# Kernel tuning notes

Hardware: AMD Instinct MI355X
Metric: run time of the kernel (lower is better)

Reference implementation:

```python
import jax, jax.numpy as jnp
import numpy as np


def _mlp(h, W_in, b_in, W_hid, b_hid, W_out, b_out):
    # 392 -> 1000 -> (1000)x4 -> 392, ReLU between linear layers (NICE shift net)
    h = jax.nn.relu(h @ W_in + b_in)
    for i in range(W_hid.shape[0]):  # fixed small layer count, not a data dim
        h = jax.nn.relu(h @ W_hid[i] + b_hid[i])
    return h @ W_out + b_out


def setup_inputs() -> dict:
    key = jax.random.key(0)
    ks = jax.random.split(key, 4)
    B, D, MID = 4096, 784, 1000
    half = D // 2
    return {
        "x": jax.random.normal(ks[0], (B, D), jnp.float32),
        "log_det_J": jnp.zeros((1,), jnp.float32),
        "W_in": jax.random.normal(ks[1], (half, MID), jnp.float32) * 0.05,
        "b_in": jnp.zeros((MID,), jnp.float32),
        "W_hid": jax.random.normal(ks[2], (4, MID, MID), jnp.float32) * 0.03,
        "b_hid": jnp.zeros((4, MID), jnp.float32),
        "W_out": jax.random.normal(ks[3], (MID, half), jnp.float32) * 0.03,
        "b_out": jnp.zeros((half,), jnp.float32),
    }


def reference(x, log_det_J, W_in, b_in, W_hid, b_hid, W_out, b_out):
    # mask_config = 0: first = even columns, second = odd columns
    first = x[:, 0::2]   # (B, D/2)
    second = x[:, 1::2]  # (B, D/2)
    shift = _mlp(first, W_in, b_in, W_hid, b_hid, W_out, b_out)
    y_second = second + shift  # coupling_law (reverse=False)
    # interleave: y[:, 0::2] = first, y[:, 1::2] = y_second, in one strided write
    y = jnp.stack([first, y_second], axis=2).reshape(x.shape)
    return (y, log_det_J)
```

## Files before the change

### kernel.cpp

```cpp
#include <hip/hip_runtime.h>

typedef __bf16 bf16;
typedef __bf16 bf16x8 __attribute__((ext_vector_type(8)));
typedef float f32x4 __attribute__((ext_vector_type(4)));

#define M_TOT 4096
#define D_IN  784
#define HALF  392
#define MID   1000
#define K0PAD 448
#define NPAD  1024
#define N5PAD 512

__device__ __forceinline__ void g2l16(const bf16* g, bf16* l) {
  __builtin_amdgcn_global_load_lds(
      (__attribute__((address_space(1))) void*)(g),
      (__attribute__((address_space(3))) void*)(l),
      16, 0, 0);
}

__global__ void prep_k(const float* __restrict__ x, const float* __restrict__ ldj,
                       const float* __restrict__ W_in, const float* __restrict__ W_hid,
                       const float* __restrict__ W_out,
                       bf16* __restrict__ A0, bf16* __restrict__ WT0,
                       bf16* __restrict__ WTh, bf16* __restrict__ WT5,
                       float* __restrict__ y) {
  int b = blockIdx.x;
  int tid = threadIdx.x;
  if (b == 0 && tid == 0) y[(size_t)M_TOT * D_IN] = ldj[0];

  if (b < 8192) {
    int m = b >> 1;
    int k = (b & 1) * 256 + tid;
    if (k < K0PAD)
      A0[(size_t)m * K0PAD + k] = (k < HALF) ? (bf16)x[(size_t)m * D_IN + 2 * k] : (bf16)0.f;
    return;
  }
  int t = b - 8192;
  const float* W; bf16* WT; int K, N, Kpad, tn, tk;
  if (t < 448) {
    W = W_in; WT = WT0; K = HALF; N = MID; Kpad = K0PAD;
    tn = t & 31; tk = t >> 5;
  } else if (t < 448 + 4096) {
    int u = t - 448; int i = u >> 10; u &= 1023;
    W = W_hid + (size_t)i * MID * MID; WT = WTh + (size_t)i * NPAD * NPAD;
    K = MID; N = MID; Kpad = NPAD;
    tn = u & 31; tk = u >> 5;
  } else {
    int u = t - 4544;
    W = W_out; WT = WT5; K = MID; N = HALF; Kpad = NPAD;
    tn = u & 15; tk = u >> 4;
  }
  __shared__ float tb[32][33];
  int n0 = tn * 32, k0 = tk * 32;
  int tx = tid & 31, ty = tid >> 5;
#pragma unroll
  for (int r = 0; r < 4; ++r) {
    int k = k0 + ty + 8 * r, n = n0 + tx;
    tb[ty + 8 * r][tx] = (k < K && n < N) ? W[(size_t)k * N + n] : 0.f;
  }
  __syncthreads();
#pragma unroll
  for (int r = 0; r < 4; ++r) {
    int n = n0 + ty + 8 * r, k = k0 + tx;
    WT[(size_t)n * Kpad + k] = (bf16)tb[tx][ty + 8 * r];
  }
}

template <int BM, int BN, int EPI, int K>
__global__ __launch_bounds__(256, 2)
void gemm_k(const bf16* __restrict__ A, const bf16* __restrict__ BT,
            const float* __restrict__ bias, int bias_n,
            bf16* __restrict__ C,
            const float* __restrict__ x, float* __restrict__ y) {
  constexpr int BK = 64;
  constexpr int MT = BM / 32, NT = BN / 32;
  constexpr int KT = K / BK;
  __shared__ bf16 ldsA[BM * BK];
  __shared__ bf16 ldsB[BN * BK];
  const int tid = threadIdx.x, wave = tid >> 6, lane = tid & 63;
  const int bn = blockIdx.x, bm = blockIdx.y;

  const int srow = lane >> 3;
  const int sq = (lane & 7) ^ srow;
  const bf16* gA = A + ((size_t)bm * BM + wave * (BM / 4) + srow) * K + sq * 8;
  const bf16* gB = BT + ((size_t)bn * BN + wave * (BN / 4) + srow) * K + sq * 8;
  bf16* lA = &ldsA[wave * (BM / 4) * BK];
  bf16* lB = &ldsB[wave * (BN / 4) * BK];

  const int mlane = lane & 15, quad = lane >> 4;
  const int wm = (wave & 1) * (BM / 2), wn = (wave >> 1) * (BN / 2);
  const int axor = mlane & 7;
  const bf16* raBase = &ldsA[(wm + mlane) * BK];
  const bf16* rbBase = &ldsB[(wn + mlane) * BK];

  f32x4 acc[MT][NT] = {};

#pragma unroll
  for (int i = 0; i < BM / 32; ++i) g2l16(gA + (size_t)(8 * i) * K, lA + (8 * i) * BK);
#pragma unroll
  for (int i = 0; i < BN / 32; ++i) g2l16(gB + (size_t)(8 * i) * K, lB + (8 * i) * BK);

  for (int kt = 0; kt < KT; ++kt) {
    __syncthreads();
    bf16x8 af[2][MT], bfr[2][NT];
#pragma unroll
    for (int s = 0; s < 2; ++s) {
      const int co = ((s * 4 + quad) ^ axor) * 8;
#pragma unroll
      for (int i = 0; i < MT; ++i) af[s][i] = *(const bf16x8*)(raBase + i * 16 * BK + co);
#pragma unroll
      for (int i = 0; i < NT; ++i) bfr[s][i] = *(const bf16x8*)(rbBase + i * 16 * BK + co);
    }
    __syncthreads();
    if (kt + 1 < KT) {
      const size_t off = (size_t)(kt + 1) * BK;
#pragma unroll
      for (int i = 0; i < BM / 32; ++i) g2l16(gA + off + (size_t)(8 * i) * K, lA + (8 * i) * BK);
#pragma unroll
      for (int i = 0; i < BN / 32; ++i) g2l16(gB + off + (size_t)(8 * i) * K, lB + (8 * i) * BK);
    }
#pragma unroll
    for (int s = 0; s < 2; ++s)
#pragma unroll
      for (int mt = 0; mt < MT; ++mt)
#pragma unroll
        for (int nt = 0; nt < NT; ++nt)
          acc[mt][nt] = __builtin_amdgcn_mfma_f32_16x16x32_bf16(
              af[s][mt], bfr[s][nt], acc[mt][nt], 0, 0, 0);
  }

  const int ng0 = bn * BN + wn + mlane;
  const int mg0 = bm * BM + wm + quad * 4;

  if (EPI == 0) {
    float bv[NT];
#pragma unroll
    for (int nt = 0; nt < NT; ++nt) {
      int n = ng0 + nt * 16;
      bv[nt] = (n < bias_n) ? bias[n] : 0.f;
    }
#pragma unroll
    for (int mt = 0; mt < MT; ++mt)
#pragma unroll
      for (int nt = 0; nt < NT; ++nt)
#pragma unroll
        for (int r = 0; r < 4; ++r) {
          int m = mg0 + mt * 16 + r;
          int n = ng0 + nt * 16;
          float v = fmaxf(acc[mt][nt][r] + bv[nt], 0.f);
          C[(size_t)m * NPAD + n] = (bf16)v;
        }
  } else {
    const float2* x2 = (const float2*)x;
    float2* y2 = (float2*)y;
#pragma unroll
    for (int nt = 0; nt < NT; ++nt) {
      int n = ng0 + nt * 16;
      if (n < HALF) {
        float bb = bias[n];
#pragma unroll
        for (int mt = 0; mt < MT; ++mt)
#pragma unroll
          for (int r = 0; r < 4; ++r) {
            int m = mg0 + mt * 16 + r;
            size_t off = (size_t)m * (D_IN / 2) + n;
            float2 v = x2[off];
            v.y += acc[mt][nt][r] + bb;
            y2[off] = v;
          }
      }
    }
  }
}

extern "C" void kernel_launch(void* const* d_in, const int* in_sizes, int n_in,
                              void* d_out, int out_size, void* d_ws, size_t ws_size,
                              hipStream_t stream) {
  const float* x     = (const float*)d_in[0];
  const float* ldj   = (const float*)d_in[1];
  const float* W_in  = (const float*)d_in[2];
  const float* b_in  = (const float*)d_in[3];
  const float* W_hid = (const float*)d_in[4];
  const float* b_hid = (const float*)d_in[5];
  const float* W_out = (const float*)d_in[6];
  const float* b_out = (const float*)d_in[7];
  float* y = (float*)d_out;

  char* p = (char*)d_ws;
  bf16* A0  = (bf16*)(p + 0);
  bf16* H0  = (bf16*)(p + 3670016);
  bf16* H1  = (bf16*)(p + 12058624);
  bf16* WT0 = (bf16*)(p + 20447232);
  bf16* WTh = (bf16*)(p + 21364736);
  bf16* WT5 = (bf16*)(p + 29753344);

  prep_k<<<dim3(8192 + 5056), 256, 0, stream>>>(x, ldj, W_in, W_hid, W_out,
                                                A0, WT0, WTh, WT5, y);

  gemm_k<64, 128, 0, K0PAD><<<dim3(8, 64), 256, 0, stream>>>(A0, WT0, b_in, MID, H0, nullptr, nullptr);
  gemm_k<64, 128, 0, NPAD><<<dim3(8, 64), 256, 0, stream>>>(H0, WTh + 0 * (size_t)NPAD * NPAD, b_hid + 0 * MID, MID, H1, nullptr, nullptr);
  gemm_k<64, 128, 0, NPAD><<<dim3(8, 64), 256, 0, stream>>>(H1, WTh + 1 * (size_t)NPAD * NPAD, b_hid + 1 * MID, MID, H0, nullptr, nullptr);
  gemm_k<64, 128, 0, NPAD><<<dim3(8, 64), 256, 0, stream>>>(H0, WTh + 2 * (size_t)NPAD * NPAD, b_hid + 2 * MID, MID, H1, nullptr, nullptr);
  gemm_k<64, 128, 0, NPAD><<<dim3(8, 64), 256, 0, stream>>>(H1, WTh + 3 * (size_t)NPAD * NPAD, b_hid + 3 * MID, MID, H0, nullptr, nullptr);
  gemm_k<64, 64, 1, NPAD><<<dim3(8, 64), 256, 0, stream>>>(H0, WT5, b_out, HALF, nullptr, x, y);
}
```

Before: 183.9 us.

## Fuse prep and six GEMM layers into one persistent kernel with row-group barriers

Replaces the prep kernel and six separate GEMM launches with a single persistent kernel of 512 blocks. Weight transposition and input packing run first, followed by a grid-wide barrier. Each later layer is separated only by an 8-block barrier over the blocks that share the same 64-row M slice, since a row tile depends only on its own rows of the previous activation. This removes launch gaps and full-grid drains between layers, but relies on all 512 blocks being co-resident, adds atomic spin barriers plus a memset launch, and loses the larger prep grid's parallelism.

```diff
diff --git a/kernel.cpp b/kernel.cpp
--- a/kernel.cpp
+++ b/kernel.cpp
@@ -10,7 +10,7 @@
 #define MID   1000
 #define K0PAD 448
 #define NPAD  1024
-#define N5PAD 512
+#define NBLK  512
 
 __device__ __forceinline__ void g2l16(const bf16* g, bf16* l) {
   __builtin_amdgcn_global_load_lds(
@@ -19,67 +19,32 @@
       16, 0, 0);
 }
 
-__global__ void prep_k(const float* __restrict__ x, const float* __restrict__ ldj,
-                       const float* __restrict__ W_in, const float* __restrict__ W_hid,
-                       const float* __restrict__ W_out,
-                       bf16* __restrict__ A0, bf16* __restrict__ WT0,
-                       bf16* __restrict__ WTh, bf16* __restrict__ WT5,
-                       float* __restrict__ y) {
-  int b = blockIdx.x;
-  int tid = threadIdx.x;
-  if (b == 0 && tid == 0) y[(size_t)M_TOT * D_IN] = ldj[0];
-
-  if (b < 8192) {
-    int m = b >> 1;
-    int k = (b & 1) * 256 + tid;
-    if (k < K0PAD)
-      A0[(size_t)m * K0PAD + k] = (k < HALF) ? (bf16)x[(size_t)m * D_IN + 2 * k] : (bf16)0.f;
-    return;
-  }
-  int t = b - 8192;
-  const float* W; bf16* WT; int K, N, Kpad, tn, tk;
-  if (t < 448) {
-    W = W_in; WT = WT0; K = HALF; N = MID; Kpad = K0PAD;
-    tn = t & 31; tk = t >> 5;
-  } else if (t < 448 + 4096) {
-    int u = t - 448; int i = u >> 10; u &= 1023;
-    W = W_hid + (size_t)i * MID * MID; WT = WTh + (size_t)i * NPAD * NPAD;
-    K = MID; N = MID; Kpad = NPAD;
-    tn = u & 31; tk = u >> 5;
-  } else {
-    int u = t - 4544;
-    W = W_out; WT = WT5; K = MID; N = HALF; Kpad = NPAD;
-    tn = u & 15; tk = u >> 4;
-  }
-  __shared__ float tb[32][33];
-  int n0 = tn * 32, k0 = tk * 32;
-  int tx = tid & 31, ty = tid >> 5;
-#pragma unroll
-  for (int r = 0; r < 4; ++r) {
-    int k = k0 + ty + 8 * r, n = n0 + tx;
-    tb[ty + 8 * r][tx] = (k < K && n < N) ? W[(size_t)k * N + n] : 0.f;
-  }
+__device__ __forceinline__ void sync_group(unsigned* cnt, unsigned* flag, unsigned nb) {
   __syncthreads();
-#pragma unroll
-  for (int r = 0; r < 4; ++r) {
-    int n = n0 + ty + 8 * r, k = k0 + tx;
-    WT[(size_t)n * Kpad + k] = (bf16)tb[tx][ty + 8 * r];
-  }
-}
-
-template <int BM, int BN, int EPI, int K>
-__global__ __launch_bounds__(256, 2)
-void gemm_k(const bf16* __restrict__ A, const bf16* __restrict__ BT,
-            const float* __restrict__ bias, int bias_n,
-            bf16* __restrict__ C,
-            const float* __restrict__ x, float* __restrict__ y) {
-  constexpr int BK = 64;
+  if (threadIdx.x == 0) {
+    __threadfence();
+    unsigned a = __hip_atomic_fetch_add(cnt, 1u, __ATOMIC_ACQ_REL, __HIP_MEMORY_SCOPE_AGENT);
+    if (a == nb - 1u) {
+      __hip_atomic_store(flag, 1u, __ATOMIC_RELEASE, __HIP_MEMORY_SCOPE_AGENT);
+    } else {
+      while (__hip_atomic_load(flag, __ATOMIC_ACQUIRE, __HIP_MEMORY_SCOPE_AGENT) == 0u)
+        __builtin_amdgcn_s_sleep(2);
+    }
+    __threadfence();
+  }
+  __syncthreads();
+}
+
+template <int K, int BN, int EPI>
+__device__ __forceinline__ void gemm_tile(
+    const bf16* __restrict__ A, const bf16* __restrict__ BT,
+    const float* __restrict__ bias, int bias_n,
+    bf16* __restrict__ C, const float* __restrict__ x, float* __restrict__ y,
+    int bm, int bn, bf16* ldsA, bf16* ldsB) {
+  constexpr int BM = 64, BK = 64;
   constexpr int MT = BM / 32, NT = BN / 32;
   constexpr int KT = K / BK;
-  __shared__ bf16 ldsA[BM * BK];
-  __shared__ bf16 ldsB[BN * BK];
   const int tid = threadIdx.x, wave = tid >> 6, lane = tid & 63;
-  const int bn = blockIdx.x, bm = blockIdx.y;
 
   const int srow = lane >> 3;
   const int sq = (lane & 7) ^ srow;
@@ -172,6 +137,84 @@
       }
     }
   }
+}
+
+__global__ __launch_bounds__(256, 2)
+void fused_k(const float* __restrict__ x, const float* __restrict__ ldj,
+             const float* __restrict__ W_in, const float* __restrict__ b_in,
+             const float* __restrict__ W_hid, const float* __restrict__ b_hid,
+             const float* __restrict__ W_out, const float* __restrict__ b_out,
+             bf16* __restrict__ A0, bf16* __restrict__ WT0,
+             bf16* __restrict__ WTh, bf16* __restrict__ WT5,
+             bf16* __restrict__ H0, bf16* __restrict__ H1,
+             float* __restrict__ y, unsigned* __restrict__ bar) {
+  __shared__ __align__(16) union {
+    struct { bf16 A[64 * 64]; bf16 B[128 * 64]; } g;
+    float tb[32][33];
+  } sm;
+  const int b = blockIdx.x, tid = threadIdx.x;
+
+  if (b == 0 && tid == 0) y[(size_t)M_TOT * D_IN] = ldj[0];
+
+#pragma unroll
+  for (int r = 0; r < 8; ++r) {
+    int m = b * 8 + r;
+    for (int k = tid; k < K0PAD; k += 256)
+      A0[(size_t)m * K0PAD + k] =
+          (k < HALF) ? (bf16)x[(size_t)m * D_IN + 2 * k] : (bf16)0.f;
+  }
+  for (int i = 0; i < 10; ++i) {
+    int t = b + i * NBLK;
+    const float* W = nullptr; bf16* WT = nullptr;
+    int K = 0, N = 0, Kpad = 0, tn = 0, tk = 0;
+    if (t < 448) {
+      W = W_in; WT = WT0; K = HALF; N = MID; Kpad = K0PAD; tn = t & 31; tk = t >> 5;
+    } else if (t < 4544) {
+      int u = t - 448, wi = u >> 10; u &= 1023;
+      W = W_hid + (size_t)wi * MID * MID; WT = WTh + (size_t)wi * NPAD * NPAD;
+      K = MID; N = MID; Kpad = NPAD; tn = u & 31; tk = u >> 5;
+    } else if (t < 5056) {
+      int u = t - 4544;
+      W = W_out; WT = WT5; K = MID; N = HALF; Kpad = NPAD; tn = u & 15; tk = u >> 4;
+    }
+    int tx = tid & 31, ty = tid >> 5;
+    if (W) {
+      int n0 = tn * 32, k0 = tk * 32;
+#pragma unroll
+      for (int r = 0; r < 4; ++r) {
+        int k = k0 + ty + 8 * r, n = n0 + tx;
+        sm.tb[ty + 8 * r][tx] = (k < K && n < N) ? W[(size_t)k * N + n] : 0.f;
+      }
+    }
+    __syncthreads();
+    if (W) {
+      int n0 = tn * 32, k0 = tk * 32;
+#pragma unroll
+      for (int r = 0; r < 4; ++r) {
+        int n = n0 + ty + 8 * r, k = k0 + tx;
+        WT[(size_t)n * Kpad + k] = (bf16)sm.tb[tx][ty + 8 * r];
+      }
+    }
+    __syncthreads();
+  }
+
+  sync_group(&bar[0], &bar[1], NBLK);
+
+  const int bm = b & 63, bn = b >> 6;
+  bf16* ldsA = sm.g.A;
+  bf16* ldsB = sm.g.B;
+
+  gemm_tile<K0PAD, 128, 0>(A0, WT0, b_in, MID, H0, nullptr, nullptr, bm, bn, ldsA, ldsB);
+  sync_group(&bar[2 + 2 * (0 * 64 + bm)], &bar[3 + 2 * (0 * 64 + bm)], 8);
+  gemm_tile<NPAD, 128, 0>(H0, WTh + 0 * (size_t)NPAD * NPAD, b_hid + 0 * MID, MID, H1, nullptr, nullptr, bm, bn, ldsA, ldsB);
+  sync_group(&bar[2 + 2 * (1 * 64 + bm)], &bar[3 + 2 * (1 * 64 + bm)], 8);
+  gemm_tile<NPAD, 128, 0>(H1, WTh + 1 * (size_t)NPAD * NPAD, b_hid + 1 * MID, MID, H0, nullptr, nullptr, bm, bn, ldsA, ldsB);
+  sync_group(&bar[2 + 2 * (2 * 64 + bm)], &bar[3 + 2 * (2 * 64 + bm)], 8);
+  gemm_tile<NPAD, 128, 0>(H0, WTh + 2 * (size_t)NPAD * NPAD, b_hid + 2 * MID, MID, H1, nullptr, nullptr, bm, bn, ldsA, ldsB);
+  sync_group(&bar[2 + 2 * (3 * 64 + bm)], &bar[3 + 2 * (3 * 64 + bm)], 8);
+  gemm_tile<NPAD, 128, 0>(H1, WTh + 3 * (size_t)NPAD * NPAD, b_hid + 3 * MID, MID, H0, nullptr, nullptr, bm, bn, ldsA, ldsB);
+  sync_group(&bar[2 + 2 * (4 * 64 + bm)], &bar[3 + 2 * (4 * 64 + bm)], 8);
+  gemm_tile<NPAD, 64, 1>(H0, WT5, b_out, HALF, nullptr, x, y, bm, bn, ldsA, ldsB);
 }
 
 extern "C" void kernel_launch(void* const* d_in, const int* in_sizes, int n_in,
@@ -188,20 +231,16 @@
   float* y = (float*)d_out;
 
   char* p = (char*)d_ws;
-  bf16* A0  = (bf16*)(p + 0);
-  bf16* H0  = (bf16*)(p + 3670016);
-  bf16* H1  = (bf16*)(p + 12058624);
-  bf16* WT0 = (bf16*)(p + 20447232);
-  bf16* WTh = (bf16*)(p + 21364736);
-  bf16* WT5 = (bf16*)(p + 29753344);
-
-  prep_k<<<dim3(8192 + 5056), 256, 0, stream>>>(x, ldj, W_in, W_hid, W_out,
-                                                A0, WT0, WTh, WT5, y);
-
-  gemm_k<64, 128, 0, K0PAD><<<dim3(8, 64), 256, 0, stream>>>(A0, WT0, b_in, MID, H0, nullptr, nullptr);
-  gemm_k<64, 128, 0, NPAD><<<dim3(8, 64), 256, 0, stream>>>(H0, WTh + 0 * (size_t)NPAD * NPAD, b_hid + 0 * MID, MID, H1, nullptr, nullptr);
-  gemm_k<64, 128, 0, NPAD><<<dim3(8, 64), 256, 0, stream>>>(H1, WTh + 1 * (size_t)NPAD * NPAD, b_hid + 1 * MID, MID, H0, nullptr, nullptr);
-  gemm_k<64, 128, 0, NPAD><<<dim3(8, 64), 256, 0, stream>>>(H0, WTh + 2 * (size_t)NPAD * NPAD, b_hid + 2 * MID, MID, H1, nullptr, nullptr);
-  gemm_k<64, 128, 0, NPAD><<<dim3(8, 64), 256, 0, stream>>>(H1, WTh + 3 * (size_t)NPAD * NPAD, b_hid + 3 * MID, MID, H0, nullptr, nullptr);
-  gemm_k<64, 64, 1, NPAD><<<dim3(8, 64), 256, 0, stream>>>(H0, WT5, b_out, HALF, nullptr, x, y);
-}
+  bf16* A0   = (bf16*)(p + 0);
+  bf16* H0   = (bf16*)(p + 3670016);
+  bf16* H1   = (bf16*)(p + 12058624);
+  bf16* WT0  = (bf16*)(p + 20447232);
+  bf16* WTh  = (bf16*)(p + 21364736);
+  bf16* WT5  = (bf16*)(p + 29753344);
+  unsigned* bar = (unsigned*)(p + 30801920);
+
+  hipMemsetAsync(bar, 0, 4096, stream);
+  fused_k<<<dim3(NBLK), 256, 0, stream>>>(x, ldj, W_in, b_in, W_hid, b_hid,
+                                          W_out, b_out, A0, WT0, WTh, WT5,
+                                          H0, H1, y, bar);
+}
```

After: 551.1 us. +199.6%, slower.
